# Kernel optimization log

Measured on AMD Instinct MI355X. Metric: run time of the kernel, lower is better.

The kernel has to match this reference:

```python
import jax, jax.numpy as jnp
import numpy as np

# Dims: batch, lig atoms (padded), rec residues, in-feat, heads, feat/head, edge-hid, n-edges
B, L, R, F, H, FH, FE, E = 16, 128, 512, 256, 8, 32, 64, 16384
HF = H * FH  # 256


def setup_inputs() -> dict:
    key = jax.random.key(0)
    ks = jax.random.split(key, 16)
    n = jax.random.normal
    return {
        "ll_feat": n(ks[0], (B, L, L, F), dtype=jnp.float32),
        "lig_feat": n(ks[1], (B, L, F), dtype=jnp.float32),
        "rec_feat": n(ks[2], (B, R, F), dtype=jnp.float32),
        "mask": jax.random.bernoulli(ks[3], 0.9, (B, L, L)),
        "e_batch": jax.random.randint(ks[4], (E,), 0, B),
        "e_src": jax.random.randint(ks[5], (E,), 0, L),
        "e_dst": jax.random.randint(ks[6], (E,), 0, L),
        # AttentionContract params: NormAndLinear (W,b + layernorm gamma/beta) + atn linear
        "Wc": n(ks[7], (HF, F)) * 0.05, "bc": jnp.zeros(HF), "gc": jnp.ones(HF), "bec": jnp.zeros(HF),
        "Wca": n(ks[8], (H, F)) * 0.05, "bca": jnp.zeros(H),
        # AttentionExpand params (x branch and y branch NormAndLinear)
        "Wex": n(ks[9], (HF, F)) * 0.05, "bex": jnp.zeros(HF), "gex": jnp.ones(HF), "beex": jnp.zeros(HF),
        "Wey": n(ks[10], (HF, F)) * 0.05, "bey": jnp.zeros(HF), "gey": jnp.ones(HF), "beey": jnp.zeros(HF),
        # edge projection (feat_to_edge_feat gather -> linear -> scatter)
        "We": n(ks[11], (FE, 2 * F)) * 0.05, "be": jnp.zeros(FE),
    }


def _norm_linear(x, W, b, g, beta):
    """NormAndLinear: linear(leaky_relu(x)) then layernorm over last dim."""
    h = jnp.einsum('...i,oi->...o', jax.nn.leaky_relu(x), W) + b
    mu = h.mean(-1, keepdims=True)
    var = ((h - mu) ** 2).mean(-1, keepdims=True)
    return g * (h - mu) * jax.lax.rsqrt(var + 1e-5) + beta


def _masked_softmax(x, mask, axis):
    """Faithful softmax_with_mask: exp(x-max), zero masked entries, /(sum+1e-10)."""
    xe = jnp.exp(x - x.max(axis=axis, keepdims=True))
    xe = jnp.where(mask, xe, 0.0)
    return xe / (xe.sum(axis=axis, keepdims=True) + 1e-10)


def reference(ll_feat, lig_feat, rec_feat, mask, e_batch, e_src, e_dst,
              Wc, bc, gc, bec, Wca, bca,
              Wex, bex, gex, beex, Wey, bey, gey, beey, We, be):
    # --- AttentionContract: (B,L,L,F) -> (B,L,H*FH), masked softmax over axis -3 (Y) ---
    of = _norm_linear(ll_feat, Wc, bc, gc, bec).reshape(B, L, L, H, FH)
    atn = (jnp.einsum('blyf,hf->blyh', jax.nn.leaky_relu(ll_feat), Wca) + bca)[..., None]  # (B,L,L,H,1)
    atn = _masked_softmax(atn, mask[..., None, None], axis=-3)
    contracted = (atn * of).sum(-3).reshape(B, L, HF)

    # --- AttentionExpand: (B,L,F),(B,R,F) -> (B,L,R,H) ---
    xf = _norm_linear(lig_feat, Wex, bex, gex, beex).reshape(B, L, H, FH)
    yf = _norm_linear(rec_feat, Wey, bey, gey, beey).reshape(B, R, H, FH)
    expanded = jnp.einsum('bxhf,byhf->bxyh', xf, yf)

    # --- feat_to_edge_feat gather + projection + lig_edges_to_ll_feat scatter ---
    ef = jnp.concatenate((lig_feat[e_batch, e_src], lig_feat[e_batch, e_dst]), axis=-1)  # (E,2F)
    ef = jax.nn.leaky_relu(ef @ We.T + be)  # (E,FE)
    llf = jnp.zeros((B, L, L, FE), ef.dtype).at[e_batch, e_src, e_dst].add(ef)

    return (contracted, expanded, llf)
```

## Files before the change

### kernel.cpp

```cpp
#include <hip/hip_runtime.h>
#include <cstdint>
#include <cstddef>

typedef unsigned int u32;
typedef unsigned short u16;
typedef __bf16 bf16x8 __attribute__((ext_vector_type(8)));
typedef float f32x16 __attribute__((ext_vector_type(16)));
typedef float f32x4v __attribute__((ext_vector_type(4)));

#define DEV static __device__ __forceinline__

DEV u16 f2bf(float f){ u32 u=__float_as_uint(f); return (u16)((u + 0x7FFFu + ((u>>16)&1u))>>16); }
DEV u32 cvtpk(float lo, float hi){ u32 r; asm("v_cvt_pk_bf16_f32 %0, %1, %2":"=v"(r):"v"(lo),"v"(hi)); return r; }
DEV uint2 cvt4(float4 v){ uint2 r; r.x=cvtpk(v.x,v.y); r.y=cvtpk(v.z,v.w); return r; }
DEV uint2 cvt4(f32x4v v){ uint2 r; r.x=cvtpk(v.x,v.y); r.y=cvtpk(v.z,v.w); return r; }
DEV u32 lrelu_pk(u32 u){
  float lo=__uint_as_float(u<<16);
  float hi=__uint_as_float(u&0xFFFF0000u);
  lo=fmaxf(lo,0.01f*lo); hi=fmaxf(hi,0.01f*hi);
  return cvtpk(lo,hi);
}

__global__ void k_prepack(const float* __restrict__ Wc, const float* __restrict__ Wca,
    const float* __restrict__ Wex, const float* __restrict__ Wey, const float* __restrict__ We,
    const unsigned char* __restrict__ maskb,
    u16* __restrict__ wpc, u16* __restrict__ wpx, u16* __restrict__ wpy,
    u16* __restrict__ wpe, int* __restrict__ flags, float* __restrict__ outl)
{
  int idx = blockIdx.x*256 + threadIdx.x;
  {
    int t=idx>>13, kk=(idx>>9)&15, ln=(idx>>3)&63, j=idx&7;
    int n=t*32+(ln&31), k=kk*16+(ln>>5)*8+j;
    if (idx < 73728){
      float v;
      if (t<8) v = Wc[n*256+k];
      else { int n2=n-256; v = (n2<8) ? Wca[n2*256+k] : 0.f; }
      wpc[idx]=f2bf(v);
    }
    if (idx < 65536){ wpx[idx]=f2bf(Wex[n*256+k]); wpy[idx]=f2bf(Wey[n*256+k]); }
  }
  if (idx < 32768){
    int t=idx>>14, kk=(idx>>9)&31, ln=(idx>>3)&63, j=idx&7;
    int n=t*32+(ln&31), k=kk*16+(ln>>5)*8+j;
    wpe[idx]=f2bf(We[n*512+k]);
  }
  {
    float4 z; z.x=0.f; z.y=0.f; z.z=0.f; z.w=0.f;
    float4* p = (float4*)outl;
    for (size_t i = (size_t)idx; i < 4194304u; i += 73728u) p[i] = z;
  }
  if (idx==0){
    int c3f1=0,c3f3=0,nzoff=0,nz4m8=0,nz0=0;
    for (int i=0;i<256;i++){
      unsigned char b=maskb[i];
      if ((i&3)==1 && b==0x3F) c3f1++;
      if ((i&3)==3 && b==0x3F) c3f3++;
      if ((i&3)!=0 && b) nzoff++;
      if ((i&7)>=4 && b) nz4m8++;
      if ((i&7)==0 && b) nz0++;
    }
    int mode;
    if (c3f1>8) mode=2;
    else if (c3f3>8) mode=3;
    else if (nzoff>8) mode=0;
    else if (nz4m8==0 && nz0>4) mode=4;
    else mode=1;
    flags[0]=mode;
  }
}

union FMem {
  struct { char slab[65536]; float maskv[128]; } c;
  struct { u16 ytile[8448]; float stage[4][2048]; } e;
  char eslab[65536];
};

DEV void contract_body(FMem& sm, int bl,
    const float* __restrict__ ll, const void* __restrict__ maskp,
    const u16* __restrict__ Wp, const float* __restrict__ bc, const float* __restrict__ bca,
    const float* __restrict__ gc, const float* __restrict__ bec,
    const int* __restrict__ flags, float* __restrict__ outc)
{
  int tid=threadIdx.x, lane=tid&63, wave=tid>>6;
  const float* src = ll + (size_t)bl*(128*256);

  if (tid < 128){
    int mode = flags[0];
    size_t mi = (size_t)bl*128 + tid;
    bool on;
    if (mode==0)      on = ((const unsigned char*)maskp)[mi] != 0;
    else if (mode==1) on = ((const int*)maskp)[mi] != 0;
    else if (mode==2) on = ((const u16*)maskp)[mi] != 0;
    else if (mode==4) on = ((const unsigned long long*)maskp)[mi] != 0ull;
    else              on = (((const u32*)maskp)[mi]<<1) != 0;
    sm.c.maskv[tid] = on ? 1.f : 0.f;
  }

  #pragma unroll 8
  for (int it=0;it<32;it++){
    int row = wave*32 + it;
    f32x4v v = __builtin_nontemporal_load((const f32x4v*)(src + row*256 + lane*4));
    uint2 pk = cvt4(v);
    *(uint2*)(sm.c.slab + row*512 + ((((lane>>1) ^ (row&31)))<<4) + (lane&1)*8) = pk;
  }

  f32x16 acc[9];
  #pragma unroll
  for (int t=0;t<9;t++)
    #pragma unroll
    for (int i=0;i<16;i++) acc[t][i]=0.f;
  int y0 = wave*32;
  int arow = y0 + (lane&31);
  int axor = arow & 31;
  int half = lane>>5;
  const char* sb = sm.c.slab;
  const u16* wl = Wp + lane*8;

  uint4 raw = *(const uint4*)(sb + arow*512 + ((half ^ axor)<<4));
  bf16x8 w0 = *(const bf16x8*)(wl);
  bf16x8 w1 = *(const bf16x8*)(wl + 8192);
  bf16x8 w2 = *(const bf16x8*)(wl + 16384);
  bf16x8 w3 = *(const bf16x8*)(wl + 24576);
  bf16x8 w4 = *(const bf16x8*)(wl + 32768);
  bf16x8 w5 = *(const bf16x8*)(wl + 40960);
  bf16x8 w6 = *(const bf16x8*)(wl + 49152);
  bf16x8 w7 = *(const bf16x8*)(wl + 57344);
  bf16x8 w8 = *(const bf16x8*)(wl + 65536);

  #pragma unroll 4
  for (int kk=0;kk<16;kk++){
    int kn = (kk+1)&15;
    uint4 rawn = *(const uint4*)(sb + arow*512 + (((kn*2+half) ^ axor)<<4));
    const u16* wkn = wl + (size_t)kn*512;
    bf16x8 n0 = *(const bf16x8*)(wkn);
    bf16x8 n1 = *(const bf16x8*)(wkn + 8192);
    bf16x8 n2 = *(const bf16x8*)(wkn + 16384);
    bf16x8 n3 = *(const bf16x8*)(wkn + 24576);
    bf16x8 n4 = *(const bf16x8*)(wkn + 32768);
    bf16x8 n5 = *(const bf16x8*)(wkn + 40960);
    bf16x8 n6 = *(const bf16x8*)(wkn + 49152);
    bf16x8 n7 = *(const bf16x8*)(wkn + 57344);
    bf16x8 n8 = *(const bf16x8*)(wkn + 65536);
    __builtin_amdgcn_sched_barrier(0);
    uint4 t4; t4.x=lrelu_pk(raw.x); t4.y=lrelu_pk(raw.y); t4.z=lrelu_pk(raw.z); t4.w=lrelu_pk(raw.w);
    bf16x8 a = __builtin_bit_cast(bf16x8, t4);
    acc[0] = __builtin_amdgcn_mfma_f32_32x32x16_bf16(a, w0, acc[0], 0,0,0);
    acc[1] = __builtin_amdgcn_mfma_f32_32x32x16_bf16(a, w1, acc[1], 0,0,0);
    acc[2] = __builtin_amdgcn_mfma_f32_32x32x16_bf16(a, w2, acc[2], 0,0,0);
    acc[3] = __builtin_amdgcn_mfma_f32_32x32x16_bf16(a, w3, acc[3], 0,0,0);
    acc[4] = __builtin_amdgcn_mfma_f32_32x32x16_bf16(a, w4, acc[4], 0,0,0);
    acc[5] = __builtin_amdgcn_mfma_f32_32x32x16_bf16(a, w5, acc[5], 0,0,0);
    acc[6] = __builtin_amdgcn_mfma_f32_32x32x16_bf16(a, w6, acc[6], 0,0,0);
    acc[7] = __builtin_amdgcn_mfma_f32_32x32x16_bf16(a, w7, acc[7], 0,0,0);
    acc[8] = __builtin_amdgcn_mfma_f32_32x32x16_bf16(a, w8, acc[8], 0,0,0);
    raw=rawn;
    w0=n0; w1=n1; w2=n2; w3=n3; w4=n4; w5=n5; w6=n6; w7=n7; w8=n8;
  }
  __syncthreads();

  float* logit = (float*)sm.c.slab;
  float* partial = logit + 1536;

  int col = lane & 31;
  float bv[8], gv[8], bev[8];
  #pragma unroll
  for (int t=0;t<8;t++){
    int n=t*32+col; bv[t]=bc[n]; gv[t]=gc[n]; bev[t]=bec[n];
  }
  float bcav = (col<8) ? bca[col] : 0.f;

  #pragma unroll
  for (int r=0;r<16;r++){
    int row=(r&3)+8*(r>>2)+4*half;
    float s=0.f, sq=0.f;
    #pragma unroll
    for (int t=0;t<8;t++){
      float v = acc[t][r] + bv[t]; acc[t][r]=v; s += v; sq = fmaf(v,v,sq);
    }
    #pragma unroll
    for (int m=1;m<=16;m<<=1){ s += __shfl_xor(s,m,64); sq += __shfl_xor(sq,m,64); }
    float mu = s*(1.f/256.f);
    float var = fmaf(sq,1.f/256.f, -mu*mu);
    float rin = rsqrtf(var+1e-5f);
    #pragma unroll
    for (int t=0;t<8;t++) acc[t][r] = fmaf((acc[t][r]-mu)*rin, gv[t], bev[t]);
    if (col<8) logit[(y0+row)*12+col] = acc[8][r] + bcav;
  }
  __syncthreads();

  {
    int h = tid>>5, sub = tid&31;
    float lv[4], ev[4];
    #pragma unroll
    for (int j=0;j<4;j++) lv[j] = logit[(sub+32*j)*12 + h];
    float mx = fmaxf(fmaxf(lv[0],lv[1]), fmaxf(lv[2],lv[3]));
    #pragma unroll
    for (int m=1;m<=16;m<<=1) mx = fmaxf(mx, __shfl_xor(mx,m,64));
    float ssum=0.f;
    #pragma unroll
    for (int j=0;j<4;j++){ ev[j] = __expf(lv[j]-mx)*sm.c.maskv[sub+32*j]; ssum += ev[j]; }
    #pragma unroll
    for (int m=1;m<=16;m<<=1) ssum += __shfl_xor(ssum,m,64);
    float inv = 1.f/(ssum+1e-10f);
    #pragma unroll
    for (int j=0;j<4;j++) logit[(sub+32*j)*12+h] = ev[j]*inv;
  }
  __syncthreads();

  float ctr[8];
  #pragma unroll
  for (int t=0;t<8;t++) ctr[t]=0.f;
  #pragma unroll
  for (int r=0;r<16;r++){
    int row=(r&3)+8*(r>>2)+4*half;
    const float* wr = &logit[(y0+row)*12];
    float4 w0v = *(const float4*)wr;
    float4 w1v = *(const float4*)(wr+4);
    ctr[0]=fmaf(w0v.x,acc[0][r],ctr[0]); ctr[1]=fmaf(w0v.y,acc[1][r],ctr[1]);
    ctr[2]=fmaf(w0v.z,acc[2][r],ctr[2]); ctr[3]=fmaf(w0v.w,acc[3][r],ctr[3]);
    ctr[4]=fmaf(w1v.x,acc[4][r],ctr[4]); ctr[5]=fmaf(w1v.y,acc[5][r],ctr[5]);
    ctr[6]=fmaf(w1v.z,acc[6][r],ctr[6]); ctr[7]=fmaf(w1v.w,acc[7][r],ctr[7]);
  }
  #pragma unroll
  for (int t=0;t<8;t++) ctr[t] += __shfl_xor(ctr[t],32,64);
  if (lane<32){
    #pragma unroll
    for (int t=0;t<8;t++) partial[wave*256 + t*32 + col] = ctr[t];
  }
  __syncthreads();
  float v = partial[tid]+partial[256+tid]+partial[512+tid]+partial[768+tid];
  outc[(size_t)bl*256 + tid] = v;
}

DEV void expand_body(FMem& sm, int blk,
    const u16* __restrict__ xf, const u16* __restrict__ yf, float* __restrict__ oute)
{
  int tid=threadIdx.x, lane=tid&63, wave=tid>>6;
  int bi = blk>>4, yt = blk&15;

  #pragma unroll
  for (int i=0;i<4;i++){
    int idx=i*256+tid; int row=idx>>5, c=idx&31;
    uint4 v = *(const uint4*)(yf + ((size_t)(bi*512 + yt*32 + row))*256 + c*8);
    *(uint4*)((char*)sm.e.ytile + row*528 + c*16) = v;
  }
  __syncthreads();

  bf16x8 af[2][8];
  #pragma unroll
  for (int xi=0;xi<2;xi++){
    int x = (wave*2+xi)*16 + (lane&15);
    #pragma unroll
    for (int h=0;h<8;h++)
      af[xi][h] = *(const bf16x8*)(xf + ((size_t)(bi*128+x))*256 + h*32 + (lane>>4)*8);
  }
  float* stw = sm.e.stage[wave];
  #pragma unroll
  for (int xi=0;xi<2;xi++){
    #pragma unroll
    for (int nt=0;nt<2;nt++){
      f32x4v c[8];
      #pragma unroll
      for (int h=0;h<8;h++){
        bf16x8 bv = *(const bf16x8*)((const char*)sm.e.ytile + (nt*16+(lane&15))*528 + (h*32+(lane>>4)*8)*2);
        f32x4v z = {0.f,0.f,0.f,0.f};
        c[h] = __builtin_amdgcn_mfma_f32_16x16x32_bf16(af[xi][h], bv, z, 0,0,0);
      }
      #pragma unroll
      for (int q=0;q<4;q++){
        int xp=(lane>>4)*4+q, yp=lane&15;
        float* sp = &stw[(xp*16+yp)*8];
        float4 v0; v0.x=c[0][q]; v0.y=c[1][q]; v0.z=c[2][q]; v0.w=c[3][q];
        float4 v1; v1.x=c[4][q]; v1.y=c[5][q]; v1.z=c[6][q]; v1.w=c[7][q];
        *(float4*)sp = v0;
        *(float4*)(sp+4) = v1;
      }
      #pragma unroll
      for (int j=0;j<4;j++){
        int pi=j*64+lane, xp=pi>>4, yp=pi&15;
        const float* sp = &stw[(xp*16+yp)*8];
        float4 a = *(const float4*)sp;
        float4 b2 = *(const float4*)(sp+4);
        size_t x=(size_t)(wave*2+xi)*16+xp, y=(size_t)yt*32+nt*16+yp;
        float* po = oute + (((size_t)bi*128+x)*512 + y)*8;
        *(float4*)po = a;
        *(float4*)(po+4) = b2;
      }
    }
  }
}

DEV void edges_body(FMem& sm, int blk,
    const float* __restrict__ lig, const int* __restrict__ eb, const int* __restrict__ es,
    const int* __restrict__ ed, const u16* __restrict__ Wp, const float* __restrict__ bias,
    float* __restrict__ outl)
{
  char* slab = sm.eslab;
  int tid=threadIdx.x, lane=tid&63, wave=tid>>6;
  int e0 = blk*64;
  int ge = e0 + wave*16 + (lane&15);
  int b0=eb[ge], s0=es[ge], d0=ed[ge];
  long long ps = (long long)(uintptr_t)(lig + ((size_t)(b0*128+s0))*256);
  long long pd = (long long)(uintptr_t)(lig + ((size_t)(b0*128+d0))*256);
  #pragma unroll 4
  for (int i=0;i<16;i++){
    int ri = wave*16 + i;
    const float* sp = (const float*)(uintptr_t)__shfl(ps, i, 16);
    const float* dp = (const float*)(uintptr_t)__shfl(pd, i, 16);
    #pragma unroll
    for (int j=0;j<2;j++){
      const float* base = j ? dp : sp;
      float4 v = *(const float4*)(base + lane*4);
      uint2 pk = cvt4(v);
      int g = j*32 + (lane>>1);
      *(uint2*)(slab + (size_t)ri*1024 + ((g ^ (ri&63))<<4) + (lane&1)*8) = pk;
    }
  }
  __syncthreads();

  f32x16 acc;
  #pragma unroll
  for (int i=0;i<16;i++) acc[i]=0.f;
  int arow = (wave&1)*32 + (lane&31);
  int axor = arow & 63;
  int half = lane>>5;
  int t = wave>>1;
  const u16* wl = Wp + lane*8 + (size_t)t*16384;

  uint4 raw = *(const uint4*)(slab + (size_t)arow*1024 + ((half ^ axor)<<4));
  bf16x8 w = *(const bf16x8*)(wl);
  for (int kk=0;kk<32;kk++){
    int kn = (kk+1)&31;
    uint4 rn = *(const uint4*)(slab + (size_t)arow*1024 + (((kn*2+half) ^ axor)<<4));
    bf16x8 nw = *(const bf16x8*)(wl + (size_t)kn*512);
    __builtin_amdgcn_sched_barrier(0);
    bf16x8 a = __builtin_bit_cast(bf16x8, raw);
    acc = __builtin_amdgcn_mfma_f32_32x32x16_bf16(a, w, acc, 0,0,0);
    raw=rn; w=nw;
  }
  int col = lane&31;
  float bv = bias[t*32+col];
  #pragma unroll
  for (int r=0;r<16;r++){
    int row=(r&3)+8*(r>>2)+4*half;
    int ee = e0 + (wave&1)*32 + row;
    int bb=eb[ee], ss=es[ee], dd=ed[ee];
    float* cell = outl + (((size_t)(bb*128+ss))*128 + (size_t)dd)*64;
    float v = acc[r] + bv;
    v = fmaxf(v, 0.01f*v);
    atomicAdd(cell + t*32 + col, v);
  }
}

__global__ __launch_bounds__(256,2) void k_fused(
    const float* __restrict__ ll, const void* __restrict__ maskp,
    const u16* __restrict__ wpc, const float* __restrict__ bc, const float* __restrict__ bca,
    const float* __restrict__ gc, const float* __restrict__ bec,
    const int* __restrict__ flags, float* __restrict__ outc,
    const u16* __restrict__ xf, const u16* __restrict__ yf, float* __restrict__ oute,
    const float* __restrict__ lig, const int* __restrict__ eb, const int* __restrict__ es,
    const int* __restrict__ ed, const u16* __restrict__ wpe, const float* __restrict__ be,
    float* __restrict__ outl)
{
  __shared__ __attribute__((aligned(16))) FMem sm;
  int bid = blockIdx.x;
  if (bid < 2048)       contract_body(sm, bid, ll, maskp, wpc, bc, bca, gc, bec, flags, outc);
  else if (bid < 2304)  expand_body(sm, bid-2048, xf, yf, oute);
  else                  edges_body(sm, bid-2304, lig, eb, es, ed, wpe, be, outl);
}

__global__ __launch_bounds__(256,2) void k_nl(
    const float* __restrict__ lig, const float* __restrict__ rec,
    const u16* __restrict__ Wpx, const u16* __restrict__ Wpy,
    const float* __restrict__ bx, const float* __restrict__ gx, const float* __restrict__ ex,
    const float* __restrict__ by, const float* __restrict__ gy, const float* __restrict__ ey,
    u16* __restrict__ xf, u16* __restrict__ yf)
{
  __shared__ __attribute__((aligned(16))) char slab[65536];
  int tid=threadIdx.x, lane=tid&63, wave=tid>>6;
  bool isx = blockIdx.x < 16;
  int bb = isx ? blockIdx.x : blockIdx.x - 16;
  const float* src  = isx ? lig : rec;
  const u16*  Wp    = isx ? Wpx : Wpy;
  const float* bias = isx ? bx : by;
  const float* g    = isx ? gx : gy;
  const float* beta = isx ? ex : ey;
  u16* dst          = isx ? xf : yf;

  const float* s0 = src + (size_t)bb*(128*256);
  #pragma unroll 8
  for (int it=0;it<32;it++){
    int row = wave*32 + it;
    float4 v = *(const float4*)(s0 + row*256 + lane*4);
    uint2 pk = cvt4(v);
    *(uint2*)(slab + row*512 + ((((lane>>1) ^ (row&31)))<<4) + (lane&1)*8) = pk;
  }

  f32x16 acc[8];
  #pragma unroll
  for (int t=0;t<8;t++)
    #pragma unroll
    for (int i=0;i<16;i++) acc[t][i]=0.f;
  int y0 = wave*32;
  int arow = y0 + (lane&31);
  int axor = arow & 31;
  int half = lane>>5;
  const u16* wl = Wp + lane*8;

  uint4 raw = *(const uint4*)(slab + arow*512 + ((half ^ axor)<<4));
  bf16x8 w0 = *(const bf16x8*)(wl);
  bf16x8 w1 = *(const bf16x8*)(wl + 8192);
  bf16x8 w2 = *(const bf16x8*)(wl + 16384);
  bf16x8 w3 = *(const bf16x8*)(wl + 24576);
  bf16x8 w4 = *(const bf16x8*)(wl + 32768);
  bf16x8 w5 = *(const bf16x8*)(wl + 40960);
  bf16x8 w6 = *(const bf16x8*)(wl + 49152);
  bf16x8 w7 = *(const bf16x8*)(wl + 57344);

  #pragma unroll 4
  for (int kk=0;kk<16;kk++){
    int kn = (kk+1)&15;
    uint4 rawn = *(const uint4*)(slab + arow*512 + (((kn*2+half) ^ axor)<<4));
    const u16* wkn = wl + (size_t)kn*512;
    bf16x8 n0 = *(const bf16x8*)(wkn);
    bf16x8 n1 = *(const bf16x8*)(wkn + 8192);
    bf16x8 n2 = *(const bf16x8*)(wkn + 16384);
    bf16x8 n3 = *(const bf16x8*)(wkn + 24576);
    bf16x8 n4 = *(const bf16x8*)(wkn + 32768);
    bf16x8 n5 = *(const bf16x8*)(wkn + 40960);
    bf16x8 n6 = *(const bf16x8*)(wkn + 49152);
    bf16x8 n7 = *(const bf16x8*)(wkn + 57344);
    __builtin_amdgcn_sched_barrier(0);
    uint4 t4; t4.x=lrelu_pk(raw.x); t4.y=lrelu_pk(raw.y); t4.z=lrelu_pk(raw.z); t4.w=lrelu_pk(raw.w);
    bf16x8 a = __builtin_bit_cast(bf16x8, t4);
    acc[0] = __builtin_amdgcn_mfma_f32_32x32x16_bf16(a, w0, acc[0], 0,0,0);
    acc[1] = __builtin_amdgcn_mfma_f32_32x32x16_bf16(a, w1, acc[1], 0,0,0);
    acc[2] = __builtin_amdgcn_mfma_f32_32x32x16_bf16(a, w2, acc[2], 0,0,0);
    acc[3] = __builtin_amdgcn_mfma_f32_32x32x16_bf16(a, w3, acc[3], 0,0,0);
    acc[4] = __builtin_amdgcn_mfma_f32_32x32x16_bf16(a, w4, acc[4], 0,0,0);
    acc[5] = __builtin_amdgcn_mfma_f32_32x32x16_bf16(a, w5, acc[5], 0,0,0);
    acc[6] = __builtin_amdgcn_mfma_f32_32x32x16_bf16(a, w6, acc[6], 0,0,0);
    acc[7] = __builtin_amdgcn_mfma_f32_32x32x16_bf16(a, w7, acc[7], 0,0,0);
    raw=rawn;
    w0=n0; w1=n1; w2=n2; w3=n3; w4=n4; w5=n5; w6=n6; w7=n7;
  }
  int col = lane & 31;
  float bv[8], gv[8], bev[8];
  #pragma unroll
  for (int t=0;t<8;t++){
    int n=t*32+col; bv[t]=bias[n]; gv[t]=g[n]; bev[t]=beta[n];
  }
  #pragma unroll
  for (int r=0;r<16;r++){
    int row=(r&3)+8*(r>>2)+4*half;
    float s=0.f, sq=0.f;
    #pragma unroll
    for (int t=0;t<8;t++){
      float v = acc[t][r] + bv[t]; acc[t][r]=v; s += v; sq = fmaf(v,v,sq);
    }
    #pragma unroll
    for (int m=1;m<=16;m<<=1){ s += __shfl_xor(s,m,64); sq += __shfl_xor(sq,m,64); }
    float mu = s*(1.f/256.f);
    float var = fmaf(sq,1.f/256.f, -mu*mu);
    float rin = rsqrtf(var+1e-5f);
    size_t rowg = (size_t)bb*128 + y0 + row;
    #pragma unroll
    for (int t=0;t<8;t++){
      float v = fmaf((acc[t][r]-mu)*rin, gv[t], bev[t]);
      dst[rowg*256 + t*32 + col] = f2bf(v);
    }
  }
}

extern "C" void kernel_launch(void* const* d_in, const int* in_sizes, int n_in,
                              void* d_out, int out_size, void* d_ws, size_t ws_size,
                              hipStream_t stream)
{
  (void)in_sizes; (void)n_in; (void)out_size; (void)ws_size;
  const float* ll  = (const float*)d_in[0];
  const float* lig = (const float*)d_in[1];
  const float* rec = (const float*)d_in[2];
  const void* mask = d_in[3];
  const int* eb = (const int*)d_in[4];
  const int* es = (const int*)d_in[5];
  const int* ed = (const int*)d_in[6];
  const float* Wc  =(const float*)d_in[7];  const float* bc  =(const float*)d_in[8];
  const float* gc  =(const float*)d_in[9];  const float* bec =(const float*)d_in[10];
  const float* Wca =(const float*)d_in[11]; const float* bca =(const float*)d_in[12];
  const float* Wex =(const float*)d_in[13]; const float* bex =(const float*)d_in[14];
  const float* gex =(const float*)d_in[15]; const float* beex=(const float*)d_in[16];
  const float* Wey =(const float*)d_in[17]; const float* bey =(const float*)d_in[18];
  const float* gey =(const float*)d_in[19]; const float* beey=(const float*)d_in[20];
  const float* We  =(const float*)d_in[21]; const float* be  =(const float*)d_in[22];

  float* outc = (float*)d_out;
  float* oute = outc + 524288;
  float* outl = outc + 8912896;

  char* ws = (char*)d_ws;
  int* flags = (int*)ws;
  u16* wpc = (u16*)(ws + 4096);
  u16* wpx = (u16*)(ws + 151552);
  u16* wpy = (u16*)(ws + 282624);
  u16* wpe = (u16*)(ws + 413696);
  u16* xf  = (u16*)(ws + 479232);
  u16* yf  = (u16*)(ws + 1527808);

  hipLaunchKernelGGL(k_prepack, dim3(288), dim3(256), 0, stream,
                     Wc, Wca, Wex, Wey, We, (const unsigned char*)mask,
                     wpc, wpx, wpy, wpe, flags, outl);
  hipLaunchKernelGGL(k_nl, dim3(80), dim3(256), 0, stream,
                     lig, rec, wpx, wpy, bex, gex, beex, bey, gey, beey, xf, yf);
  hipLaunchKernelGGL(k_fused, dim3(2560), dim3(256), 0, stream,
                     ll, mask, wpc, bc, bca, gc, bec, flags, outc,
                     xf, yf, oute, lig, eb, es, ed, wpe, be, outl);
}
```

Baseline: 510.6 us.

## Process four contract rows per block with double-buffered LDS prefetch

```diff
diff --git a/kernel.cpp b/kernel.cpp
--- a/kernel.cpp
+++ b/kernel.cpp
@@ -70,166 +70,242 @@
 }
 
 union FMem {
-  struct { char slab[65536]; float maskv[128]; } c;
+  struct {
+    char buf[2][32768];
+    float logit[1536];
+    float partial[1024];
+    float maskv[128];
+  } c;
   struct { u16 ytile[8448]; float stage[4][2048]; } e;
   char eslab[65536];
 };
 
-DEV void contract_body(FMem& sm, int bl,
+DEV void contract4_body(FMem& sm, int blk4,
     const float* __restrict__ ll, const void* __restrict__ maskp,
     const u16* __restrict__ Wp, const float* __restrict__ bc, const float* __restrict__ bca,
     const float* __restrict__ gc, const float* __restrict__ bec,
     const int* __restrict__ flags, float* __restrict__ outc)
 {
   int tid=threadIdx.x, lane=tid&63, wave=tid>>6;
-  const float* src = ll + (size_t)bl*(128*256);
-
-  if (tid < 128){
-    int mode = flags[0];
-    size_t mi = (size_t)bl*128 + tid;
-    bool on;
-    if (mode==0)      on = ((const unsigned char*)maskp)[mi] != 0;
-    else if (mode==1) on = ((const int*)maskp)[mi] != 0;
-    else if (mode==2) on = ((const u16*)maskp)[mi] != 0;
-    else if (mode==4) on = ((const unsigned long long*)maskp)[mi] != 0ull;
-    else              on = (((const u32*)maskp)[mi]<<1) != 0;
-    sm.c.maskv[tid] = on ? 1.f : 0.f;
-  }
-
-  #pragma unroll 8
-  for (int it=0;it<32;it++){
-    int row = wave*32 + it;
-    f32x4v v = __builtin_nontemporal_load((const f32x4v*)(src + row*256 + lane*4));
-    uint2 pk = cvt4(v);
-    *(uint2*)(sm.c.slab + row*512 + ((((lane>>1) ^ (row&31)))<<4) + (lane&1)*8) = pk;
-  }
-
-  f32x16 acc[9];
-  #pragma unroll
-  for (int t=0;t<9;t++)
-    #pragma unroll
-    for (int i=0;i<16;i++) acc[t][i]=0.f;
-  int y0 = wave*32;
-  int arow = y0 + (lane&31);
-  int axor = arow & 31;
-  int half = lane>>5;
-  const char* sb = sm.c.slab;
+  int rl = lane&31, half = lane>>5, y0 = wave*32;
   const u16* wl = Wp + lane*8;
-
-  uint4 raw = *(const uint4*)(sb + arow*512 + ((half ^ axor)<<4));
-  bf16x8 w0 = *(const bf16x8*)(wl);
-  bf16x8 w1 = *(const bf16x8*)(wl + 8192);
-  bf16x8 w2 = *(const bf16x8*)(wl + 16384);
-  bf16x8 w3 = *(const bf16x8*)(wl + 24576);
-  bf16x8 w4 = *(const bf16x8*)(wl + 32768);
-  bf16x8 w5 = *(const bf16x8*)(wl + 40960);
-  bf16x8 w6 = *(const bf16x8*)(wl + 49152);
-  bf16x8 w7 = *(const bf16x8*)(wl + 57344);
-  bf16x8 w8 = *(const bf16x8*)(wl + 65536);
-
-  #pragma unroll 4
-  for (int kk=0;kk<16;kk++){
-    int kn = (kk+1)&15;
-    uint4 rawn = *(const uint4*)(sb + arow*512 + (((kn*2+half) ^ axor)<<4));
-    const u16* wkn = wl + (size_t)kn*512;
-    bf16x8 n0 = *(const bf16x8*)(wkn);
-    bf16x8 n1 = *(const bf16x8*)(wkn + 8192);
-    bf16x8 n2 = *(const bf16x8*)(wkn + 16384);
-    bf16x8 n3 = *(const bf16x8*)(wkn + 24576);
-    bf16x8 n4 = *(const bf16x8*)(wkn + 32768);
-    bf16x8 n5 = *(const bf16x8*)(wkn + 40960);
-    bf16x8 n6 = *(const bf16x8*)(wkn + 49152);
-    bf16x8 n7 = *(const bf16x8*)(wkn + 57344);
-    bf16x8 n8 = *(const bf16x8*)(wkn + 65536);
-    __builtin_amdgcn_sched_barrier(0);
-    uint4 t4; t4.x=lrelu_pk(raw.x); t4.y=lrelu_pk(raw.y); t4.z=lrelu_pk(raw.z); t4.w=lrelu_pk(raw.w);
-    bf16x8 a = __builtin_bit_cast(bf16x8, t4);
-    acc[0] = __builtin_amdgcn_mfma_f32_32x32x16_bf16(a, w0, acc[0], 0,0,0);
-    acc[1] = __builtin_amdgcn_mfma_f32_32x32x16_bf16(a, w1, acc[1], 0,0,0);
-    acc[2] = __builtin_amdgcn_mfma_f32_32x32x16_bf16(a, w2, acc[2], 0,0,0);
-    acc[3] = __builtin_amdgcn_mfma_f32_32x32x16_bf16(a, w3, acc[3], 0,0,0);
-    acc[4] = __builtin_amdgcn_mfma_f32_32x32x16_bf16(a, w4, acc[4], 0,0,0);
-    acc[5] = __builtin_amdgcn_mfma_f32_32x32x16_bf16(a, w5, acc[5], 0,0,0);
-    acc[6] = __builtin_amdgcn_mfma_f32_32x32x16_bf16(a, w6, acc[6], 0,0,0);
-    acc[7] = __builtin_amdgcn_mfma_f32_32x32x16_bf16(a, w7, acc[7], 0,0,0);
-    acc[8] = __builtin_amdgcn_mfma_f32_32x32x16_bf16(a, w8, acc[8], 0,0,0);
-    raw=rawn;
-    w0=n0; w1=n1; w2=n2; w3=n3; w4=n4; w5=n5; w6=n6; w7=n7; w8=n8;
-  }
-  __syncthreads();
-
-  float* logit = (float*)sm.c.slab;
-  float* partial = logit + 1536;
-
-  int col = lane & 31;
-  float bv[8], gv[8], bev[8];
-  #pragma unroll
-  for (int t=0;t<8;t++){
-    int n=t*32+col; bv[t]=bc[n]; gv[t]=gc[n]; bev[t]=bec[n];
-  }
-  float bcav = (col<8) ? bca[col] : 0.f;
-
-  #pragma unroll
-  for (int r=0;r<16;r++){
-    int row=(r&3)+8*(r>>2)+4*half;
-    float s=0.f, sq=0.f;
+  int mode = flags[0];
+
+  char* wb0 = sm.c.buf[0] + wave*8192;
+  char* wb1 = sm.c.buf[1] + wave*8192;
+  const float* llb = ll + (size_t)blk4*(4*128*256) + (size_t)(y0+half)*256 + rl*4;
+
+#define STW(dst, i, sv) { int rw_=(i)*2+half; uint2 pk_; \
+    pk_.x=cvtpk((sv)[0],(sv)[1]); pk_.y=cvtpk((sv)[2],(sv)[3]); \
+    *(uint2*)((dst) + rw_*256 + ((((rl>>1) ^ (rw_&15)))<<4) + (rl&1)*8) = pk_; }
+
+  {
+    const float* s = llb;
+    f32x4v s0,s1,s2,s3,s4,s5,s6,s7;
+    s0=__builtin_nontemporal_load((const f32x4v*)(s+0*512));
+    s1=__builtin_nontemporal_load((const f32x4v*)(s+1*512));
+    s2=__builtin_nontemporal_load((const f32x4v*)(s+2*512));
+    s3=__builtin_nontemporal_load((const f32x4v*)(s+3*512));
+    s4=__builtin_nontemporal_load((const f32x4v*)(s+4*512));
+    s5=__builtin_nontemporal_load((const f32x4v*)(s+5*512));
+    s6=__builtin_nontemporal_load((const f32x4v*)(s+6*512));
+    s7=__builtin_nontemporal_load((const f32x4v*)(s+7*512));
+    STW(wb0,0,s0); STW(wb0,1,s1); STW(wb0,2,s2); STW(wb0,3,s3);
+    STW(wb0,4,s4); STW(wb0,5,s5); STW(wb0,6,s6); STW(wb0,7,s7);
+    s0=__builtin_nontemporal_load((const f32x4v*)(s+8*512));
+    s1=__builtin_nontemporal_load((const f32x4v*)(s+9*512));
+    s2=__builtin_nontemporal_load((const f32x4v*)(s+10*512));
+    s3=__builtin_nontemporal_load((const f32x4v*)(s+11*512));
+    s4=__builtin_nontemporal_load((const f32x4v*)(s+12*512));
+    s5=__builtin_nontemporal_load((const f32x4v*)(s+13*512));
+    s6=__builtin_nontemporal_load((const f32x4v*)(s+14*512));
+    s7=__builtin_nontemporal_load((const f32x4v*)(s+15*512));
+    STW(wb0,8,s0); STW(wb0,9,s1); STW(wb0,10,s2); STW(wb0,11,s3);
+    STW(wb0,12,s4); STW(wb0,13,s5); STW(wb0,14,s6); STW(wb0,15,s7);
+  }
+
+  for (int tt=0; tt<4; ++tt){
+    f32x16 acc[9];
+    #pragma unroll
+    for (int t=0;t<9;t++)
+      #pragma unroll
+      for (int i=0;i<16;i++) acc[t][i]=0.f;
+
+    #pragma unroll
+    for (int hk=0; hk<2; ++hk){
+      int p = tt*2 + hk;
+      const char* rb = (p&1) ? wb1 : wb0;
+      char* wn       = (p&1) ? wb0 : wb1;
+      bool has_next = (p < 7);
+      int tn = (p+1)>>1, hn = (p+1)&1;
+      const float* sn = llb + (size_t)tn*(128*256) + hn*128;
+
+      f32x4v s0,s1,s2,s3,s4,s5,s6,s7;
+      if (has_next){
+        s0=__builtin_nontemporal_load((const f32x4v*)(sn+0*512));
+        s1=__builtin_nontemporal_load((const f32x4v*)(sn+1*512));
+        s2=__builtin_nontemporal_load((const f32x4v*)(sn+2*512));
+        s3=__builtin_nontemporal_load((const f32x4v*)(sn+3*512));
+        s4=__builtin_nontemporal_load((const f32x4v*)(sn+4*512));
+        s5=__builtin_nontemporal_load((const f32x4v*)(sn+5*512));
+        s6=__builtin_nontemporal_load((const f32x4v*)(sn+6*512));
+        s7=__builtin_nontemporal_load((const f32x4v*)(sn+7*512));
+      }
+      #pragma unroll
+      for (int k=0;k<4;k++){
+        uint4 raw = *(const uint4*)(rb + rl*256 + ((((k*2+half)) ^ (rl&15))<<4));
+        const u16* wk = wl + (size_t)(hk*8+k)*512;
+        bf16x8 b0 = *(const bf16x8*)(wk);
+        bf16x8 b1 = *(const bf16x8*)(wk + 8192);
+        bf16x8 b2 = *(const bf16x8*)(wk + 16384);
+        bf16x8 b3 = *(const bf16x8*)(wk + 24576);
+        bf16x8 b4 = *(const bf16x8*)(wk + 32768);
+        bf16x8 b5 = *(const bf16x8*)(wk + 40960);
+        bf16x8 b6 = *(const bf16x8*)(wk + 49152);
+        bf16x8 b7 = *(const bf16x8*)(wk + 57344);
+        bf16x8 b8 = *(const bf16x8*)(wk + 65536);
+        __builtin_amdgcn_sched_barrier(0);
+        uint4 t4; t4.x=lrelu_pk(raw.x); t4.y=lrelu_pk(raw.y); t4.z=lrelu_pk(raw.z); t4.w=lrelu_pk(raw.w);
+        bf16x8 a = __builtin_bit_cast(bf16x8, t4);
+        acc[0] = __builtin_amdgcn_mfma_f32_32x32x16_bf16(a, b0, acc[0], 0,0,0);
+        acc[1] = __builtin_amdgcn_mfma_f32_32x32x16_bf16(a, b1, acc[1], 0,0,0);
+        acc[2] = __builtin_amdgcn_mfma_f32_32x32x16_bf16(a, b2, acc[2], 0,0,0);
+        acc[3] = __builtin_amdgcn_mfma_f32_32x32x16_bf16(a, b3, acc[3], 0,0,0);
+        acc[4] = __builtin_amdgcn_mfma_f32_32x32x16_bf16(a, b4, acc[4], 0,0,0);
+        acc[5] = __builtin_amdgcn_mfma_f32_32x32x16_bf16(a, b5, acc[5], 0,0,0);
+        acc[6] = __builtin_amdgcn_mfma_f32_32x32x16_bf16(a, b6, acc[6], 0,0,0);
+        acc[7] = __builtin_amdgcn_mfma_f32_32x32x16_bf16(a, b7, acc[7], 0,0,0);
+        acc[8] = __builtin_amdgcn_mfma_f32_32x32x16_bf16(a, b8, acc[8], 0,0,0);
+      }
+      if (has_next){
+        STW(wn,0,s0); STW(wn,1,s1); STW(wn,2,s2); STW(wn,3,s3);
+        STW(wn,4,s4); STW(wn,5,s5); STW(wn,6,s6); STW(wn,7,s7);
+        s0=__builtin_nontemporal_load((const f32x4v*)(sn+8*512));
+        s1=__builtin_nontemporal_load((const f32x4v*)(sn+9*512));
+        s2=__builtin_nontemporal_load((const f32x4v*)(sn+10*512));
+        s3=__builtin_nontemporal_load((const f32x4v*)(sn+11*512));
+        s4=__builtin_nontemporal_load((const f32x4v*)(sn+12*512));
+        s5=__builtin_nontemporal_load((const f32x4v*)(sn+13*512));
+        s6=__builtin_nontemporal_load((const f32x4v*)(sn+14*512));
+        s7=__builtin_nontemporal_load((const f32x4v*)(sn+15*512));
+      }
+      #pragma unroll
+      for (int k=4;k<8;k++){
+        uint4 raw = *(const uint4*)(rb + rl*256 + ((((k*2+half)) ^ (rl&15))<<4));
+        const u16* wk = wl + (size_t)(hk*8+k)*512;
+        bf16x8 b0 = *(const bf16x8*)(wk);
+        bf16x8 b1 = *(const bf16x8*)(wk + 8192);
+        bf16x8 b2 = *(const bf16x8*)(wk + 16384);
+        bf16x8 b3 = *(const bf16x8*)(wk + 24576);
+        bf16x8 b4 = *(const bf16x8*)(wk + 32768);
+        bf16x8 b5 = *(const bf16x8*)(wk + 40960);
+        bf16x8 b6 = *(const bf16x8*)(wk + 49152);
+        bf16x8 b7 = *(const bf16x8*)(wk + 57344);
+        bf16x8 b8 = *(const bf16x8*)(wk + 65536);
+        __builtin_amdgcn_sched_barrier(0);
+        uint4 t4; t4.x=lrelu_pk(raw.x); t4.y=lrelu_pk(raw.y); t4.z=lrelu_pk(raw.z); t4.w=lrelu_pk(raw.w);
+        bf16x8 a = __builtin_bit_cast(bf16x8, t4);
+        acc[0] = __builtin_amdgcn_mfma_f32_32x32x16_bf16(a, b0, acc[0], 0,0,0);
+        acc[1] = __builtin_amdgcn_mfma_f32_32x32x16_bf16(a, b1, acc[1], 0,0,0);
+        acc[2] = __builtin_amdgcn_mfma_f32_32x32x16_bf16(a, b2, acc[2], 0,0,0);
+        acc[3] = __builtin_amdgcn_mfma_f32_32x32x16_bf16(a, b3, acc[3], 0,0,0);
+        acc[4] = __builtin_amdgcn_mfma_f32_32x32x16_bf16(a, b4, acc[4], 0,0,0);
+        acc[5] = __builtin_amdgcn_mfma_f32_32x32x16_bf16(a, b5, acc[5], 0,0,0);
+        acc[6] = __builtin_amdgcn_mfma_f32_32x32x16_bf16(a, b6, acc[6], 0,0,0);
+        acc[7] = __builtin_amdgcn_mfma_f32_32x32x16_bf16(a, b7, acc[7], 0,0,0);
+        acc[8] = __builtin_amdgcn_mfma_f32_32x32x16_bf16(a, b8, acc[8], 0,0,0);
+      }
+      if (has_next){
+        STW(wn,8,s0); STW(wn,9,s1); STW(wn,10,s2); STW(wn,11,s3);
+        STW(wn,12,s4); STW(wn,13,s5); STW(wn,14,s6); STW(wn,15,s7);
+      }
+    }
+
+    int bl = blk4*4 + tt;
+    if (tid < 128){
+      size_t mi = (size_t)bl*128 + tid;
+      bool on;
+      if (mode==0)      on = ((const unsigned char*)maskp)[mi] != 0;
+      else if (mode==1) on = ((const int*)maskp)[mi] != 0;
+      else if (mode==2) on = ((const u16*)maskp)[mi] != 0;
+      else if (mode==4) on = ((const unsigned long long*)maskp)[mi] != 0ull;
+      else              on = (((const u32*)maskp)[mi]<<1) != 0;
+      sm.c.maskv[tid] = on ? 1.f : 0.f;
+    }
+    float* logit = sm.c.logit;
+    float* partial = sm.c.partial;
+    int col = lane & 31;
+    float bv[8], gv[8], bev[8];
     #pragma unroll
     for (int t=0;t<8;t++){
-      float v = acc[t][r] + bv[t]; acc[t][r]=v; s += v; sq = fmaf(v,v,sq);
-    }
-    #pragma unroll
-    for (int m=1;m<=16;m<<=1){ s += __shfl_xor(s,m,64); sq += __shfl_xor(sq,m,64); }
-    float mu = s*(1.f/256.f);
-    float var = fmaf(sq,1.f/256.f, -mu*mu);
-    float rin = rsqrtf(var+1e-5f);
-    #pragma unroll
-    for (int t=0;t<8;t++) acc[t][r] = fmaf((acc[t][r]-mu)*rin, gv[t], bev[t]);
-    if (col<8) logit[(y0+row)*12+col] = acc[8][r] + bcav;
-  }
-  __syncthreads();
-
-  {
-    int h = tid>>5, sub = tid&31;
-    float lv[4], ev[4];
-    #pragma unroll
-    for (int j=0;j<4;j++) lv[j] = logit[(sub+32*j)*12 + h];
-    float mx = fmaxf(fmaxf(lv[0],lv[1]), fmaxf(lv[2],lv[3]));
-    #pragma unroll
-    for (int m=1;m<=16;m<<=1) mx = fmaxf(mx, __shfl_xor(mx,m,64));
-    float ssum=0.f;
-    #pragma unroll
-    for (int j=0;j<4;j++){ ev[j] = __expf(lv[j]-mx)*sm.c.maskv[sub+32*j]; ssum += ev[j]; }
-    #pragma unroll
-    for (int m=1;m<=16;m<<=1) ssum += __shfl_xor(ssum,m,64);
-    float inv = 1.f/(ssum+1e-10f);
-    #pragma unroll
-    for (int j=0;j<4;j++) logit[(sub+32*j)*12+h] = ev[j]*inv;
-  }
-  __syncthreads();
-
-  float ctr[8];
-  #pragma unroll
-  for (int t=0;t<8;t++) ctr[t]=0.f;
-  #pragma unroll
-  for (int r=0;r<16;r++){
-    int row=(r&3)+8*(r>>2)+4*half;
-    const float* wr = &logit[(y0+row)*12];
-    float4 w0v = *(const float4*)wr;
-    float4 w1v = *(const float4*)(wr+4);
-    ctr[0]=fmaf(w0v.x,acc[0][r],ctr[0]); ctr[1]=fmaf(w0v.y,acc[1][r],ctr[1]);
-    ctr[2]=fmaf(w0v.z,acc[2][r],ctr[2]); ctr[3]=fmaf(w0v.w,acc[3][r],ctr[3]);
-    ctr[4]=fmaf(w1v.x,acc[4][r],ctr[4]); ctr[5]=fmaf(w1v.y,acc[5][r],ctr[5]);
-    ctr[6]=fmaf(w1v.z,acc[6][r],ctr[6]); ctr[7]=fmaf(w1v.w,acc[7][r],ctr[7]);
-  }
-  #pragma unroll
-  for (int t=0;t<8;t++) ctr[t] += __shfl_xor(ctr[t],32,64);
-  if (lane<32){
-    #pragma unroll
-    for (int t=0;t<8;t++) partial[wave*256 + t*32 + col] = ctr[t];
-  }
-  __syncthreads();
-  float v = partial[tid]+partial[256+tid]+partial[512+tid]+partial[768+tid];
-  outc[(size_t)bl*256 + tid] = v;
+      int n=t*32+col; bv[t]=bc[n]; gv[t]=gc[n]; bev[t]=bec[n];
+    }
+    float bcav = (col<8) ? bca[col] : 0.f;
+
+    #pragma unroll
+    for (int r=0;r<16;r++){
+      int row=(r&3)+8*(r>>2)+4*half;
+      float s=0.f, sq=0.f;
+      #pragma unroll
+      for (int t=0;t<8;t++){
+        float v = acc[t][r] + bv[t]; acc[t][r]=v; s += v; sq = fmaf(v,v,sq);
+      }
+      #pragma unroll
+      for (int m=1;m<=16;m<<=1){ s += __shfl_xor(s,m,64); sq += __shfl_xor(sq,m,64); }
+      float mu = s*(1.f/256.f);
+      float var = fmaf(sq,1.f/256.f, -mu*mu);
+      float rin = rsqrtf(var+1e-5f);
+      #pragma unroll
+      for (int t=0;t<8;t++) acc[t][r] = fmaf((acc[t][r]-mu)*rin, gv[t], bev[t]);
+      if (col<8) logit[(y0+row)*12+col] = acc[8][r] + bcav;
+    }
+    __syncthreads();
+
+    {
+      int h = tid>>5, sub = tid&31;
+      float lv[4], ev[4];
+      #pragma unroll
+      for (int j=0;j<4;j++) lv[j] = logit[(sub+32*j)*12 + h];
+      float mx = fmaxf(fmaxf(lv[0],lv[1]), fmaxf(lv[2],lv[3]));
+      #pragma unroll
+      for (int m=1;m<=16;m<<=1) mx = fmaxf(mx, __shfl_xor(mx,m,64));
+      float ssum=0.f;
+      #pragma unroll
+      for (int j=0;j<4;j++){ ev[j] = __expf(lv[j]-mx)*sm.c.maskv[sub+32*j]; ssum += ev[j]; }
+      #pragma unroll
+      for (int m=1;m<=16;m<<=1) ssum += __shfl_xor(ssum,m,64);
+      float inv = 1.f/(ssum+1e-10f);
+      #pragma unroll
+      for (int j=0;j<4;j++) logit[(sub+32*j)*12+h] = ev[j]*inv;
+    }
+    __syncthreads();
+
+    float ctr[8];
+    #pragma unroll
+    for (int t=0;t<8;t++) ctr[t]=0.f;
+    #pragma unroll
+    for (int r=0;r<16;r++){
+      int row=(r&3)+8*(r>>2)+4*half;
+      const float* wr = &logit[(y0+row)*12];
+      float4 w0v = *(const float4*)wr;
+      float4 w1v = *(const float4*)(wr+4);
+      ctr[0]=fmaf(w0v.x,acc[0][r],ctr[0]); ctr[1]=fmaf(w0v.y,acc[1][r],ctr[1]);
+      ctr[2]=fmaf(w0v.z,acc[2][r],ctr[2]); ctr[3]=fmaf(w0v.w,acc[3][r],ctr[3]);
+      ctr[4]=fmaf(w1v.x,acc[4][r],ctr[4]); ctr[5]=fmaf(w1v.y,acc[5][r],ctr[5]);
+      ctr[6]=fmaf(w1v.z,acc[6][r],ctr[6]); ctr[7]=fmaf(w1v.w,acc[7][r],ctr[7]);
+    }
+    #pragma unroll
+    for (int t=0;t<8;t++) ctr[t] += __shfl_xor(ctr[t],32,64);
+    if (lane<32){
+      #pragma unroll
+      for (int t=0;t<8;t++) partial[wave*256 + t*32 + col] = ctr[t];
+    }
+    __syncthreads();
+    float v = partial[tid]+partial[256+tid]+partial[512+tid]+partial[768+tid];
+    outc[(size_t)bl*256 + tid] = v;
+    __syncthreads();
+  }
+#undef STW
 }
 
 DEV void expand_body(FMem& sm, int blk,
@@ -364,9 +440,13 @@
 {
   __shared__ __attribute__((aligned(16))) FMem sm;
   int bid = blockIdx.x;
-  if (bid < 2048)       contract_body(sm, bid, ll, maskp, wpc, bc, bca, gc, bec, flags, outc);
-  else if (bid < 2304)  expand_body(sm, bid-2048, xf, yf, oute);
-  else                  edges_body(sm, bid-2304, lig, eb, es, ed, wpe, be, outl);
+  if (bid & 1){
+    int j = bid>>1;
+    if (j < 256) expand_body(sm, j, xf, yf, oute);
+    else         edges_body(sm, j-256, lig, eb, es, ed, wpe, be, outl);
+  } else {
+    contract4_body(sm, bid>>1, ll, maskp, wpc, bc, bca, gc, bec, flags, outc);
+  }
 }
 
 __global__ __launch_bounds__(256,2) void k_nl(
@@ -511,7 +591,7 @@
                      wpc, wpx, wpy, wpe, flags, outl);
   hipLaunchKernelGGL(k_nl, dim3(80), dim3(256), 0, stream,
                      lig, rec, wpx, wpy, bex, gex, beex, bey, gey, beey, xf, yf);
-  hipLaunchKernelGGL(k_fused, dim3(2560), dim3(256), 0, stream,
+  hipLaunchKernelGGL(k_fused, dim3(1024), dim3(256), 0, stream,
                      ll, mask, wpc, bc, bca, gc, bec, flags, outc,
                      xf, yf, oute, lig, eb, es, ed, wpe, be, outl);
 }
```

Measured after the change: 938.6 us. 1.84x slower.
